# Kernel tuning notes

Hardware: AMD Instinct MI355X
Metric: run time of the kernel (lower is better)

The kernel has to match this reference:

```python
import jax, jax.numpy as jnp
import numpy as np

G = 64  # fixed grid size hardcoded in the torch module

def setup_inputs() -> dict:
    key = jax.random.key(0)
    ks = jax.random.split(key, 12)
    N, H = 500000, 256
    s = lambda fan_in: 1.0 / np.sqrt(fan_in)
    return {
        "positions": jax.random.normal(ks[0], (N, 3), jnp.float32) * 2.0,
        "grid_points": jax.random.normal(ks[1], (G, 3), jnp.float32) * 2.0,
        "W1": jax.random.normal(ks[2], (3, 64), jnp.float32) * s(3),
        "b1": jnp.zeros((64,), jnp.float32),
        "W2": jax.random.normal(ks[3], (64, 128), jnp.float32) * s(64),
        "b2": jnp.zeros((128,), jnp.float32),
        "W3": jax.random.normal(ks[4], (128, H), jnp.float32) * s(128),
        "b3": jnp.zeros((H,), jnp.float32),
        "Wn1": jax.random.normal(ks[5], (H, H), jnp.float32) * s(H),
        "bn1": jnp.zeros((H,), jnp.float32),
        "Wn2": jax.random.normal(ks[6], (H, H), jnp.float32) * s(H),
        "bn2": jnp.zeros((H,), jnp.float32),
        "Wh1": jax.random.normal(ks[7], (4, H, 128), jnp.float32) * s(H),
        "bh1": jnp.zeros((4, 128), jnp.float32),
        "Wh2": jax.random.normal(ks[8], (4, 128, 1), jnp.float32) * s(128),
        "bh2": jnp.zeros((4, 1), jnp.float32),
    }

def reference(positions, grid_points, W1, b1, W2, b2, W3, b3,
              Wn1, bn1, Wn2, bn2, Wh1, bh1, Wh2, bh2):
    # crystal_encoder: per-atom MLP 3 -> 64 -> 128 -> 256 over ALL N atoms
    h = jax.nn.relu(positions @ W1 + b1)
    h = jax.nn.relu(h @ W2 + b2)
    feat = h @ W3 + b3                                   # [N, H]

    # _map_crystal_to_grid: only the first min(N, 64) atoms are mapped.
    pos64 = positions[:G]                                # [64, 3]
    d2 = jnp.sum((pos64[:, None, :] - grid_points[None, :, :]) ** 2, axis=-1)
    idx = jnp.argmin(d2, axis=-1)                        # [64] nearest grid point per atom
    winner = jnp.full((G,), -1, jnp.int32).at[idx].max(jnp.arange(G, dtype=jnp.int32))
    grid_feats = jnp.where(winner[:, None] >= 0,
                           feat[jnp.clip(winner, 0)], 0.0)  # [64, H]

    # TetrahedralAGINetwork (per-node MLP, channels-first output convention)
    x = grid_feats[None]                                 # [1, 64, H]
    y = jax.nn.relu(x @ Wn1 + bn1) @ Wn2 + bn2           # [1, 64, H]
    agg = jnp.mean(jnp.swapaxes(y, 1, 2), axis=-1)       # mean over nodes -> [1, H]

    # 4 property heads, batched: [4, 1, 1] -> [4] (order: band_gap,
    # elastic_modulus, thermal_conductivity, dielectric_constant)
    h1 = jax.nn.relu(jnp.einsum('bc,kcd->kbd', agg, Wh1) + bh1[:, None, :])
    props = jnp.einsum('kbd,kdo->kbo', h1, Wh2) + bh2[:, None, :]
    return props.reshape(4)
```

## Files before the change

kernel.cpp:

```cpp
#include <hip/hip_runtime.h>


__device__ __forceinline__ void async_cp16(const float* g, float* l) {
    __builtin_amdgcn_global_load_lds(
        (const __attribute__((address_space(1))) void*)g,
        (__attribute__((address_space(3))) void*)l, 16, 0, 0);
}
__device__ __forceinline__ void stage_contig(const float* g, float* l, int nfloats, int tid) {
    const int lane = tid & 63, wv = tid >> 6;
    const int ninst = nfloats >> 8;
    for (int i = wv; i < ninst; i += 4)
        async_cp16(g + i*256 + lane*4, l + i*256);
}
__device__ __forceinline__ void stage_slice32(const float* g, float* l, int ld, int j0, int nrows, int tid) {
    const int lane = tid & 63, wv = tid >> 6;
    const int r = lane >> 3, c4 = (lane & 7) << 2;
    const int ninst = nrows >> 3;
    for (int i = wv; i < ninst; i += 4)
        async_cp16(g + (i*8 + r)*ld + j0 + c4, l + i*256);
}

#define AB_SMEM_BYTES (32768*4)

__global__ __launch_bounds__(256) void ab_fused(
    const float* __restrict__ positions, const float* __restrict__ grid_pts,
    const float* __restrict__ W1, const float* __restrict__ b1,
    const float* __restrict__ W2, const float* __restrict__ b2,
    const float* __restrict__ W3, const float* __restrict__ b3,
    const float* __restrict__ Wn1, const float* __restrict__ bn1,
    float* __restrict__ tpart_ws)
{
    extern __shared__ float sm[];
    __shared__ float pos_s[192], grid_s[192], w1_s[192], b1_s[64];
    __shared__ int   idx_s[64], win_s[8];
    __shared__ __align__(16) float h1s[8*64];
    __shared__ __align__(16) float h2s[8*128];
    __shared__ __align__(16) float gf_s[8*256];
    __shared__ float r_s[256];

    const int tid = threadIdx.x;
    const int blk = blockIdx.x;
    const int bg  = blk >> 3;

    stage_contig(W3, sm, 32768, tid);
    if (tid < 192) { pos_s[tid] = positions[tid]; grid_s[tid] = grid_pts[tid]; w1_s[tid] = W1[tid]; }
    if (tid >= 192) b1_s[tid - 192] = b1[tid - 192];
    const float bb2 = b2[tid & 127];
    const float bb3 = b3[tid];
    __syncthreads();

    if (tid < 64) {
        const float px = pos_s[tid*3], py = pos_s[tid*3+1], pz = pos_s[tid*3+2];
        float best = 3.4e38f; int bi = 0;
        for (int g = 0; g < 64; ++g) {
            const float dx = px - grid_s[g*3];
            const float dy = py - grid_s[g*3+1];
            const float dz = pz - grid_s[g*3+2];
            const float d2 = dx*dx + dy*dy + dz*dz;
            if (d2 < best) { best = d2; bi = g; }
        }
        idx_s[tid] = bi;
    }
    __syncthreads();
    if (tid < 8) {
        const int g = bg*8 + tid;
        int m = -1;
        for (int i = 0; i < 64; ++i) if (idx_s[i] == g) m = i;
        win_s[tid] = m;
    }
    __syncthreads();

    #pragma unroll
    for (int u = 0; u < 2; ++u) {
        const int e  = tid + u*256;
        const int lr = e >> 6, kk = e & 63;
        int r = win_s[lr]; if (r < 0) r = 0;
        const float acc = b1_s[kk] + pos_s[r*3]*w1_s[kk] + pos_s[r*3+1]*w1_s[64+kk]
                                   + pos_s[r*3+2]*w1_s[128+kk];
        h1s[lr*64 + kk] = fmaxf(acc, 0.f);
    }
    __syncthreads();

    {
        const int d = tid & 127, t0 = tid >> 7;
        float acc[4];
        #pragma unroll
        for (int m = 0; m < 4; ++m) acc[m] = bb2;
        for (int kc = 0; kc < 64; kc += 16) {
            float w[16];
            #pragma unroll
            for (int u = 0; u < 16; ++u) w[u] = W2[(kc+u)*128 + d];
            #pragma unroll
            for (int u = 0; u < 16; u += 4) {
                #pragma unroll
                for (int m = 0; m < 4; ++m) {
                    const float4 h4 = *(const float4*)&h1s[(t0 + 2*m)*64 + kc + u];
                    acc[m] += h4.x*w[u] + h4.y*w[u+1] + h4.z*w[u+2] + h4.w*w[u+3];
                }
            }
        }
        #pragma unroll
        for (int m = 0; m < 4; ++m)
            h2s[(t0 + 2*m)*128 + d] = fmaxf(acc[m], 0.f);
    }
    __syncthreads();

    {
        const int j = tid;
        float ag[8];
        #pragma unroll
        for (int t = 0; t < 8; ++t) ag[t] = 0.f;
        for (int dc = 0; dc < 128; dc += 16) {
            float w[16];
            #pragma unroll
            for (int u = 0; u < 16; ++u) w[u] = sm[(dc+u)*256 + j];
            #pragma unroll
            for (int u = 0; u < 16; u += 4) {
                #pragma unroll
                for (int t = 0; t < 8; ++t) {
                    const float4 h4 = *(const float4*)&h2s[t*128 + dc + u];
                    ag[t] += h4.x*w[u] + h4.y*w[u+1] + h4.z*w[u+2] + h4.w*w[u+3];
                }
            }
        }
        #pragma unroll
        for (int t = 0; t < 8; ++t)
            gf_s[t*256 + j] = (win_s[t] >= 0) ? (ag[t] + bb3) : 0.f;
    }
    __syncthreads();

    {
        const int j0 = (blk & 7) * 32;
        stage_slice32(Wn1, sm, 256, j0, 256, tid);
        const int jl = tid & 31, t = tid >> 5;
        const float bb = bn1[j0 + jl];
        __syncthreads();

        float acc = bb;
        for (int cc = 0; cc < 256; cc += 32) {
            float w[32];
            #pragma unroll
            for (int u = 0; u < 32; ++u) w[u] = sm[(cc+u)*32 + jl];
            #pragma unroll
            for (int u = 0; u < 32; u += 4) {
                const float4 g4 = *(const float4*)&gf_s[t*256 + cc + u];
                acc += g4.x*w[u] + g4.y*w[u+1] + g4.z*w[u+2] + g4.w*w[u+3];
            }
        }
        r_s[tid] = fmaxf(acc, 0.f);
        __syncthreads();
        if (t == 0) {
            float ps = 0.f;
            #pragma unroll
            for (int tt = 0; tt < 8; ++tt) ps += r_s[tt*32 + jl];
            tpart_ws[bg*256 + j0 + jl] = ps;
        }
    }
}

#define CD_SMEM_BYTES (32768*4)

__global__ __launch_bounds__(256) void cd_head(
    const float* __restrict__ Wn2, const float* __restrict__ bn2,
    const float* __restrict__ Wh1, const float* __restrict__ bh1,
    const float* __restrict__ Wh2, const float* __restrict__ bh2,
    const float* __restrict__ tpart_ws,
    float* __restrict__ out)
{
    extern __shared__ float sm[];
    __shared__ __align__(16) float tp_s[2048];
    __shared__ __align__(16) float tbar_s[256];
    __shared__ __align__(16) float agg_s[256];
    __shared__ __align__(16) float h1h_s[128];
    __shared__ __align__(16) float wh2_s[128];

    float* bufA = sm;
    float* bufB = sm + 16384;

    const int tid = threadIdx.x;
    const int k   = blockIdx.x;

    stage_contig(tpart_ws, tp_s, 2048, tid);
    stage_contig(Wn2,          bufA, 16384, tid);
    stage_contig(Wn2 + 16384,  bufB, 16384, tid);
    const float bbn2  = bn2[tid];
    const float bbh1k = (tid < 128) ? bh1[k*128 + tid] : 0.f;
    if (tid < 128) wh2_s[tid] = Wh2[k*128 + tid];
    const float bbh2k = bh2[k];
    __syncthreads();

    {
        float tb = 0.f;
        #pragma unroll
        for (int q = 0; q < 8; ++q) tb += tp_s[q*256 + tid];
        tbar_s[tid] = tb * (1.f/64.f);
    }
    __syncthreads();

    float acc = bbn2;
    for (int jc = 0; jc < 64; jc += 32) {
        float w[32];
        #pragma unroll
        for (int u = 0; u < 32; ++u) w[u] = bufA[(jc+u)*256 + tid];
        #pragma unroll
        for (int u = 0; u < 32; u += 4) {
            const float4 t4 = *(const float4*)&tbar_s[jc + u];
            acc += t4.x*w[u] + t4.y*w[u+1] + t4.z*w[u+2] + t4.w*w[u+3];
        }
    }
    __syncthreads();
    stage_contig(Wn2 + 32768, bufA, 16384, tid);
    for (int jc = 64; jc < 128; jc += 32) {
        float w[32];
        #pragma unroll
        for (int u = 0; u < 32; ++u) w[u] = bufB[(jc-64+u)*256 + tid];
        #pragma unroll
        for (int u = 0; u < 32; u += 4) {
            const float4 t4 = *(const float4*)&tbar_s[jc + u];
            acc += t4.x*w[u] + t4.y*w[u+1] + t4.z*w[u+2] + t4.w*w[u+3];
        }
    }
    __syncthreads();
    stage_contig(Wn2 + 49152, bufB, 16384, tid);
    for (int jc = 128; jc < 192; jc += 32) {
        float w[32];
        #pragma unroll
        for (int u = 0; u < 32; ++u) w[u] = bufA[(jc-128+u)*256 + tid];
        #pragma unroll
        for (int u = 0; u < 32; u += 4) {
            const float4 t4 = *(const float4*)&tbar_s[jc + u];
            acc += t4.x*w[u] + t4.y*w[u+1] + t4.z*w[u+2] + t4.w*w[u+3];
        }
    }
    __syncthreads();
    for (int jc = 192; jc < 256; jc += 32) {
        float w[32];
        #pragma unroll
        for (int u = 0; u < 32; ++u) w[u] = bufB[(jc-192+u)*256 + tid];
        #pragma unroll
        for (int u = 0; u < 32; u += 4) {
            const float4 t4 = *(const float4*)&tbar_s[jc + u];
            acc += t4.x*w[u] + t4.y*w[u+1] + t4.z*w[u+2] + t4.w*w[u+3];
        }
    }
    agg_s[tid] = acc;
    __syncthreads();
    stage_contig(Wh1 + k*32768,         bufA, 16384, tid);
    stage_contig(Wh1 + k*32768 + 16384, bufB, 16384, tid);
    __syncthreads();

    if (tid < 128) {
        const int d = tid;
        float a = bbh1k;
        for (int cc = 0; cc < 128; cc += 16) {
            float wa[16];
            #pragma unroll
            for (int u = 0; u < 16; ++u) wa[u] = bufA[(cc+u)*128 + d];
            #pragma unroll
            for (int u = 0; u < 16; u += 4) {
                const float4 a4 = *(const float4*)&agg_s[cc + u];
                a += a4.x*wa[u] + a4.y*wa[u+1] + a4.z*wa[u+2] + a4.w*wa[u+3];
            }
        }
        for (int cc = 128; cc < 256; cc += 16) {
            float wa[16];
            #pragma unroll
            for (int u = 0; u < 16; ++u) wa[u] = bufB[(cc-128+u)*128 + d];
            #pragma unroll
            for (int u = 0; u < 16; u += 4) {
                const float4 a4 = *(const float4*)&agg_s[cc + u];
                a += a4.x*wa[u] + a4.y*wa[u+1] + a4.z*wa[u+2] + a4.w*wa[u+3];
            }
        }
        h1h_s[d] = fmaxf(a, 0.f);
    }
    __syncthreads();
    if (tid == 0) {
        float a = bbh2k;
        for (int d = 0; d < 128; ++d) a += h1h_s[d] * wh2_s[d];
        out[k] = a;
    }
}

extern "C" void kernel_launch(void* const* d_in, const int* in_sizes, int n_in,
                              void* d_out, int out_size, void* d_ws, size_t ws_size,
                              hipStream_t stream) {
    const float* positions = (const float*)d_in[0];
    const float* grid      = (const float*)d_in[1];
    const float* W1  = (const float*)d_in[2];
    const float* b1  = (const float*)d_in[3];
    const float* W2  = (const float*)d_in[4];
    const float* b2  = (const float*)d_in[5];
    const float* W3  = (const float*)d_in[6];
    const float* b3  = (const float*)d_in[7];
    const float* Wn1 = (const float*)d_in[8];
    const float* bn1 = (const float*)d_in[9];
    const float* Wn2 = (const float*)d_in[10];
    const float* bn2 = (const float*)d_in[11];
    const float* Wh1 = (const float*)d_in[12];
    const float* bh1 = (const float*)d_in[13];
    const float* Wh2 = (const float*)d_in[14];
    const float* bh2 = (const float*)d_in[15];
    float* out = (float*)d_out;

    float* tpart_ws = (float*)d_ws;

    (void)hipFuncSetAttribute((const void*)ab_fused,
                              hipFuncAttributeMaxDynamicSharedMemorySize,
                              AB_SMEM_BYTES);
    (void)hipFuncSetAttribute((const void*)cd_head,
                              hipFuncAttributeMaxDynamicSharedMemorySize,
                              CD_SMEM_BYTES);

    hipLaunchKernelGGL(ab_fused, dim3(64), dim3(256), AB_SMEM_BYTES, stream,
                       positions, grid, W1, b1, W2, b2, W3, b3, Wn1, bn1, tpart_ws);
    hipLaunchKernelGGL(cd_head,  dim3(4),  dim3(256), CD_SMEM_BYTES, stream,
                       Wn2, bn2, Wh1, bh1, Wh2, bh2, tpart_ws, out);
}
```

Measured before the change: 109.9 us.

## Fuse encoder and head kernels into one launch with atomic-counter grid sync

Merges the two kernels into a single 64-block launch. Blocks publish completion through global atomic counters, and designated blocks spin-wait on them. The Wn2 aggregation matvec is spread across 32 blocks of 8 columns each, and the 4 head blocks prefetch Wh1 while waiting. The aim is to remove the second kernel launch and its serialized single-block Wn2 pass. In exchange it adds a memset launch, depends on all blocks being co-resident, and has a bounded spin guard that could silently produce wrong results if it times out.

```diff
diff --git a/kernel.cpp b/kernel.cpp
--- a/kernel.cpp
+++ b/kernel.cpp
@@ -20,15 +20,21 @@
         async_cp16(g + (i*8 + r)*ld + j0 + c4, l + i*256);
 }
 
-#define AB_SMEM_BYTES (32768*4)
-
-__global__ __launch_bounds__(256) void ab_fused(
+#define F_SMEM_BYTES (32768*4)
+
+__global__ __launch_bounds__(256) void fused_all(
     const float* __restrict__ positions, const float* __restrict__ grid_pts,
     const float* __restrict__ W1, const float* __restrict__ b1,
     const float* __restrict__ W2, const float* __restrict__ b2,
     const float* __restrict__ W3, const float* __restrict__ b3,
     const float* __restrict__ Wn1, const float* __restrict__ bn1,
-    float* __restrict__ tpart_ws)
+    const float* __restrict__ Wn2, const float* __restrict__ bn2,
+    const float* __restrict__ Wh1, const float* __restrict__ bh1,
+    const float* __restrict__ Wh2, const float* __restrict__ bh2,
+    float* __restrict__ tpart_ws,
+    float* __restrict__ agg_ws,
+    unsigned int* __restrict__ cnts,
+    float* __restrict__ out)
 {
     extern __shared__ float sm[];
     __shared__ float pos_s[192], grid_s[192], w1_s[192], b1_s[64];
@@ -37,6 +43,11 @@
     __shared__ __align__(16) float h2s[8*128];
     __shared__ __align__(16) float gf_s[8*256];
     __shared__ float r_s[256];
+    __shared__ __align__(16) float tp_s[2048];
+    __shared__ __align__(16) float tbar_s[256];
+    __shared__ __align__(16) float agg_s[256];
+    __shared__ __align__(16) float h1h_s[128];
+    __shared__ __align__(16) float wh2_s[128];
 
     const int tid = threadIdx.x;
     const int blk = blockIdx.x;
@@ -156,98 +167,79 @@
             tpart_ws[bg*256 + j0 + jl] = ps;
         }
     }
-}
-
-#define CD_SMEM_BYTES (32768*4)
-
-__global__ __launch_bounds__(256) void cd_head(
-    const float* __restrict__ Wn2, const float* __restrict__ bn2,
-    const float* __restrict__ Wh1, const float* __restrict__ bh1,
-    const float* __restrict__ Wh2, const float* __restrict__ bh2,
-    const float* __restrict__ tpart_ws,
-    float* __restrict__ out)
-{
-    extern __shared__ float sm[];
-    __shared__ __align__(16) float tp_s[2048];
-    __shared__ __align__(16) float tbar_s[256];
-    __shared__ __align__(16) float agg_s[256];
-    __shared__ __align__(16) float h1h_s[128];
-    __shared__ __align__(16) float wh2_s[128];
+
+    const bool is_head = (blk < 4);
+    const bool is_agg  = (blk >= 8 && blk < 40);
+    if (is_head) {
+        stage_contig(Wh1 + blk*32768, sm, 32768, tid);
+        if (tid < 128) wh2_s[tid] = Wh2[blk*128 + tid];
+    } else if (is_agg) {
+        const int j0a = (blk - 8) * 8;
+        const int lane = tid & 63, wv = tid >> 6;
+        const int r = lane >> 1, c4 = (lane & 1) << 2;
+        for (int i = wv; i < 8; i += 4)
+            async_cp16(Wn2 + (i*32 + r)*256 + j0a + c4, sm + i*256);
+    }
+    __syncthreads();
+    if (tid == 0)
+        __hip_atomic_fetch_add(&cnts[0], 1u, __ATOMIC_RELEASE, __HIP_MEMORY_SCOPE_AGENT);
+
+    if (is_agg) {
+        if (tid == 0) {
+            unsigned guard = 0;
+            while (__hip_atomic_load(&cnts[0], __ATOMIC_ACQUIRE, __HIP_MEMORY_SCOPE_AGENT) < 64u) {
+                if (++guard > (1u << 24)) break;
+            }
+        }
+        __syncthreads();
+        stage_contig(tpart_ws, tp_s, 2048, tid);
+        __syncthreads();
+
+        {
+            float tb = 0.f;
+            #pragma unroll
+            for (int q = 0; q < 8; ++q) tb += tp_s[q*256 + tid];
+            tbar_s[tid] = tb * (1.f/64.f);
+        }
+        __syncthreads();
+
+        if (tid < 8) {
+            const int j0a = (blk - 8) * 8;
+            float acc = bn2[j0a + tid];
+            for (int jc = 0; jc < 256; jc += 32) {
+                float w[32];
+                #pragma unroll
+                for (int u = 0; u < 32; ++u) w[u] = sm[(jc+u)*8 + tid];
+                #pragma unroll
+                for (int u = 0; u < 32; u += 4) {
+                    const float4 t4 = *(const float4*)&tbar_s[jc + u];
+                    acc += t4.x*w[u] + t4.y*w[u+1] + t4.z*w[u+2] + t4.w*w[u+3];
+                }
+            }
+            agg_ws[j0a + tid] = acc;
+        }
+        __syncthreads();
+        if (tid == 0)
+            __hip_atomic_fetch_add(&cnts[1], 1u, __ATOMIC_RELEASE, __HIP_MEMORY_SCOPE_AGENT);
+        return;
+    }
+    if (!is_head) return;
+
+    const int k = blk;
+    const float bbh1k = (tid < 128) ? bh1[k*128 + tid] : 0.f;
+    const float bbh2k = bh2[k];
+    if (tid == 0) {
+        unsigned guard = 0;
+        while (__hip_atomic_load(&cnts[1], __ATOMIC_ACQUIRE, __HIP_MEMORY_SCOPE_AGENT) < 32u) {
+            if (++guard > (1u << 24)) break;
+        }
+    }
+    __syncthreads();
+    agg_s[tid] = agg_ws[tid];
+    __syncthreads();
 
     float* bufA = sm;
     float* bufB = sm + 16384;
-
-    const int tid = threadIdx.x;
-    const int k   = blockIdx.x;
-
-    stage_contig(tpart_ws, tp_s, 2048, tid);
-    stage_contig(Wn2,          bufA, 16384, tid);
-    stage_contig(Wn2 + 16384,  bufB, 16384, tid);
-    const float bbn2  = bn2[tid];
-    const float bbh1k = (tid < 128) ? bh1[k*128 + tid] : 0.f;
-    if (tid < 128) wh2_s[tid] = Wh2[k*128 + tid];
-    const float bbh2k = bh2[k];
-    __syncthreads();
-
-    {
-        float tb = 0.f;
-        #pragma unroll
-        for (int q = 0; q < 8; ++q) tb += tp_s[q*256 + tid];
-        tbar_s[tid] = tb * (1.f/64.f);
-    }
-    __syncthreads();
-
-    float acc = bbn2;
-    for (int jc = 0; jc < 64; jc += 32) {
-        float w[32];
-        #pragma unroll
-        for (int u = 0; u < 32; ++u) w[u] = bufA[(jc+u)*256 + tid];
-        #pragma unroll
-        for (int u = 0; u < 32; u += 4) {
-            const float4 t4 = *(const float4*)&tbar_s[jc + u];
-            acc += t4.x*w[u] + t4.y*w[u+1] + t4.z*w[u+2] + t4.w*w[u+3];
-        }
-    }
-    __syncthreads();
-    stage_contig(Wn2 + 32768, bufA, 16384, tid);
-    for (int jc = 64; jc < 128; jc += 32) {
-        float w[32];
-        #pragma unroll
-        for (int u = 0; u < 32; ++u) w[u] = bufB[(jc-64+u)*256 + tid];
-        #pragma unroll
-        for (int u = 0; u < 32; u += 4) {
-            const float4 t4 = *(const float4*)&tbar_s[jc + u];
-            acc += t4.x*w[u] + t4.y*w[u+1] + t4.z*w[u+2] + t4.w*w[u+3];
-        }
-    }
-    __syncthreads();
-    stage_contig(Wn2 + 49152, bufB, 16384, tid);
-    for (int jc = 128; jc < 192; jc += 32) {
-        float w[32];
-        #pragma unroll
-        for (int u = 0; u < 32; ++u) w[u] = bufA[(jc-128+u)*256 + tid];
-        #pragma unroll
-        for (int u = 0; u < 32; u += 4) {
-            const float4 t4 = *(const float4*)&tbar_s[jc + u];
-            acc += t4.x*w[u] + t4.y*w[u+1] + t4.z*w[u+2] + t4.w*w[u+3];
-        }
-    }
-    __syncthreads();
-    for (int jc = 192; jc < 256; jc += 32) {
-        float w[32];
-        #pragma unroll
-        for (int u = 0; u < 32; ++u) w[u] = bufB[(jc-192+u)*256 + tid];
-        #pragma unroll
-        for (int u = 0; u < 32; u += 4) {
-            const float4 t4 = *(const float4*)&tbar_s[jc + u];
-            acc += t4.x*w[u] + t4.y*w[u+1] + t4.z*w[u+2] + t4.w*w[u+3];
-        }
-    }
-    agg_s[tid] = acc;
-    __syncthreads();
-    stage_contig(Wh1 + k*32768,         bufA, 16384, tid);
-    stage_contig(Wh1 + k*32768 + 16384, bufB, 16384, tid);
-    __syncthreads();
 
     if (tid < 128) {
         const int d = tid;
@@ -301,19 +293,21 @@
     const float* bh1 = (const float*)d_in[13];
     const float* Wh2 = (const float*)d_in[14];
     const float* bh2 = (const float*)d_in[15];
-    float* out = (float*)d_out;
-
-    float* tpart_ws = (float*)d_ws;
-
-    (void)hipFuncSetAttribute((const void*)ab_fused,
+    float* outp = (float*)d_out;
+
+    char* ws = (char*)d_ws;
+    float* tpart_ws = (float*)(ws + 0);
+    float* agg_ws   = (float*)(ws + 8192);
+    unsigned int* cnts = (unsigned int*)(ws + 10240);
+
+    (void)hipMemsetAsync((void*)cnts, 0, 16, stream);
+
+    (void)hipFuncSetAttribute((const void*)fused_all,
                               hipFuncAttributeMaxDynamicSharedMemorySize,
-                              AB_SMEM_BYTES);
-    (void)hipFuncSetAttribute((const void*)cd_head,
-                              hipFuncAttributeMaxDynamicSharedMemorySize,
-                              CD_SMEM_BYTES);
-
-    hipLaunchKernelGGL(ab_fused, dim3(64), dim3(256), AB_SMEM_BYTES, stream,
-                       positions, grid, W1, b1, W2, b2, W3, b3, Wn1, bn1, tpart_ws);
-    hipLaunchKernelGGL(cd_head,  dim3(4),  dim3(256), CD_SMEM_BYTES, stream,
-                       Wn2, bn2, Wh1, bh1, Wh2, bh2, tpart_ws, out);
-}
+                              F_SMEM_BYTES);
+
+    hipLaunchKernelGGL(fused_all, dim3(64), dim3(256), F_SMEM_BYTES, stream,
+                       positions, grid, W1, b1, W2, b2, W3, b3, Wn1, bn1,
+                       Wn2, bn2, Wh1, bh1, Wh2, bh2,
+                       tpart_ws, agg_ws, cnts, outp);
+}
```

Result: slower. 114.4 us (+4.1%).
